# Kernel tuning notes

Measured on AMD Instinct MI355X. Metric: run time of the kernel, lower is better.

Reference implementation:

```python
import jax, jax.numpy as jnp
import numpy as np

IN = 128; HID = 128; OUT = 128; HEADS = 3; T1 = 0.2; T2 = 0.2
B = 512; L = 32; V = 100000; NMETA = 5


def _corr_full(s, t):
    # s, t: (B, L, E, N). Full cross-correlation along last axis.
    # Matches F.conv1d(hs, ht, groups=BLE, padding=N-1): out[k] = sum_m s[k+m-(N-1)] * t[m]
    N = s.shape[-1]
    sp = jnp.pad(s, ((0, 0), (0, 0), (0, 0), (N - 1, N - 1)))
    out = jnp.stack([(sp[..., k:k + N] * t).sum(-1) for k in range(2 * N - 1)], axis=-1)
    return jnp.swapaxes(out, -1, -2)  # (B, L, 2N-1, E)


def _node_att(h, Wt, Ws, Wc):
    # h: (B, L, P, E); Wt/Ws/Wc: (HEADS, E, HID)
    Bh, Lh, P, E = h.shape
    H = h.reshape(Bh * Lh, P, E)
    hi = jnp.einsum('ne,heo->hno', H[:, 0], Wt)                 # target-node projection
    logits = jnp.einsum('npe,heo,hno->hnp', H, Ws, hi) / T1     # (heads, BL, P)
    alpha = jax.nn.softmax(logits, axis=-1)                     # softmax over path positions
    Z = jnp.einsum('hnp,npe,heo->no', alpha, H, Wc) / HEADS     # mean over heads
    return Z.reshape(Bh, Lh, -1)


def _forward(emb_user, emb_item, emb_attr1, emb_attr2, emb_attr3, Wt, Ws, Wc,
             pw1, pb1, pw2, fw1, fb1, fw2, fb2,
             UI, IU, UIUI, IUIU, UIAI1, IAIU1, UIAI2, IAIU2, UIAI3, IAIU3):
    src = emb_user[UI[:, 0, 0]]
    tgt = emb_item[IU[:, 0, 0]]
    ui = jnp.stack([emb_user[UI[..., 0]], emb_item[UI[..., 1]]], axis=3)
    iu = jnp.stack([emb_item[IU[..., 0]], emb_user[IU[..., 1]]], axis=3)

    def p4(tabs, idx):
        return jnp.stack([tabs[k][idx[..., k]] for k in range(4)], axis=3)

    uiui = p4([emb_user, emb_item, emb_user, emb_item], UIUI)
    iuiu = p4([emb_item, emb_user, emb_item, emb_user], IUIU)
    uiai1 = p4([emb_user, emb_item, emb_attr1, emb_item], UIAI1)
    iaiu1 = p4([emb_item, emb_attr1, emb_item, emb_user], IAIU1)
    uiai2 = p4([emb_user, emb_item, emb_attr2, emb_item], UIAI2)
    iaiu2 = p4([emb_item, emb_attr2, emb_item, emb_user], IAIU2)
    uiai3 = p4([emb_user, emb_item, emb_attr3, emb_item], UIAI3)
    iaiu3 = p4([emb_item, emb_attr3, emb_item, emb_user], IAIU3)

    user_feats = [ui, uiui, uiai1, uiai2, uiai3]
    item_feats = [iu, iuiu, iaiu1, iaiu2, iaiu3]
    Hs = [_node_att(_corr_full(uf, itf), Wt[m], Ws[m], Wc[m])
          for m, (uf, itf) in enumerate(zip(user_feats, item_feats))]
    Z = jnp.stack(Hs, 1)                        # (B, 5, L, HID)
    z = Z.reshape(Z.shape[0], -1, HID)          # (B, 5L, HID)
    w = jnp.tanh(z @ pw1 + pb1) @ pw2 / T2      # (B, 5L, 1)
    beta = jax.nn.softmax(w, axis=1)
    path_out = (beta * z).sum(1)                # (B, HID)
    x = jnp.concatenate([src, tgt, path_out], axis=1)
    x = jax.nn.relu(x @ fw1 + fb1)              # dropout in eval mode -> identity
    return jax.nn.sigmoid(x @ fw2 + fb2)        # (B, 1)


def setup_inputs() -> dict:
    key = jax.random.key(0)
    ks = jax.random.split(key, 24)

    def idx(k, n):
        return jax.random.randint(k, (B, L, n), 0, V, dtype=jnp.int32)

    d = {
        'UI': idx(ks[0], 2), 'IU': idx(ks[1], 2),
        'UIUI': idx(ks[2], 4), 'IUIU': idx(ks[3], 4),
        'UIAI1': idx(ks[4], 4), 'IAIU1': idx(ks[5], 4),
        'UIAI2': idx(ks[6], 4), 'IAIU2': idx(ks[7], 4),
        'UIAI3': idx(ks[8], 4), 'IAIU3': idx(ks[9], 4),
    }

    def emb(k):
        t = jax.random.normal(k, (V + 1, IN), jnp.float32) * 0.05
        return t.at[0].set(0.0)  # padding_idx=0

    d['emb_user'] = emb(ks[10]); d['emb_item'] = emb(ks[11])
    d['emb_attr1'] = emb(ks[12]); d['emb_attr2'] = emb(ks[13]); d['emb_attr3'] = emb(ks[14])
    s = (2.0 / (IN + HID)) ** 0.5  # xavier scale
    d['Wt'] = jax.random.normal(ks[15], (NMETA, HEADS, IN, HID), jnp.float32) * s
    d['Ws'] = jax.random.normal(ks[16], (NMETA, HEADS, IN, HID), jnp.float32) * s
    d['Wc'] = jax.random.normal(ks[17], (NMETA, HEADS, IN, HID), jnp.float32) * s
    d['pw1'] = jax.random.normal(ks[18], (HID, HID), jnp.float32) * s
    d['pb1'] = jnp.zeros((HID,), jnp.float32)
    d['pw2'] = jax.random.normal(ks[19], (HID, 1), jnp.float32) * s
    d['fw1'] = jax.random.normal(ks[20], (3 * HID, OUT), jnp.float32) * 0.02
    d['fb1'] = jnp.zeros((OUT,), jnp.float32)
    d['fw2'] = jax.random.normal(ks[21], (OUT, 1), jnp.float32) * 0.02
    d['fb2'] = jnp.zeros((1,), jnp.float32)
    return d


def reference(UI, IU, UIUI, IUIU, UIAI1, IAIU1, UIAI2, IAIU2, UIAI3, IAIU3,
              emb_user, emb_item, emb_attr1, emb_attr2, emb_attr3,
              Wt, Ws, Wc, pw1, pb1, pw2, fw1, fb1, fw2, fb2):
    return _forward(emb_user, emb_item, emb_attr1, emb_attr2, emb_attr3, Wt, Ws, Wc,
                    pw1, pb1, pw2, fw1, fb1, fw2, fb2,
                    UI, IU, UIUI, IUIU, UIAI1, IAIU1, UIAI2, IAIU2, UIAI3, IAIU3)
```

## Files before the change

### kernel.cpp

```cpp
#include <hip/hip_runtime.h>
#include <hip/hip_bf16.h>
#include <cstdint>
#include <cstddef>


typedef __hip_bfloat16 bf16;
typedef __attribute__((ext_vector_type(8))) short  bfrag;
typedef __attribute__((ext_vector_type(4))) float  ffrag;

__device__ __forceinline__ float bflo(uint32_t u) { return __uint_as_float(u << 16); }
__device__ __forceinline__ float bfhi(uint32_t u) { return __uint_as_float(u & 0xffff0000u); }
__device__ __forceinline__ float bfs(unsigned short s) {
  return __uint_as_float(((uint32_t)s) << 16);
}
__device__ __forceinline__ uint16_t f2bfu(float x) {
  bf16 h = __float2bfloat16(x);
  return *(uint16_t*)&h;
}
__device__ __forceinline__ uint32_t pk2(float lo, float hi) {
  return (uint32_t)f2bfu(lo) | ((uint32_t)f2bfu(hi) << 16);
}

__global__ __launch_bounds__(256) void conv_emb(
    const float* __restrict__ a, const float* __restrict__ b,
    ushort* __restrict__ da, ushort* __restrict__ db, int n4)
{
  int stride = gridDim.x * 256;
  for (int i = blockIdx.x * 256 + threadIdx.x; i < 2 * n4; i += stride) {
    const float4* s; ushort* d; int j;
    if (i < n4) { s = (const float4*)a; d = da; j = i; }
    else        { s = (const float4*)b; d = db; j = i - n4; }
    float4 v = s[j];
    ushort4 o;
    o.x = f2bfu(v.x); o.y = f2bfu(v.y); o.z = f2bfu(v.z); o.w = f2bfu(v.w);
    ((ushort4*)d)[j] = o;
  }
}

__global__ __launch_bounds__(256) void prep_all(
    const float* __restrict__ Ws, const float* __restrict__ Wt,
    const float* __restrict__ Wc, const float* __restrict__ pw1,
    bf16* __restrict__ BmT, bf16* __restrict__ WcT, bf16* __restrict__ pw1T)
{
  int bid = blockIdx.x;
  int tid = threadIdx.x;
  if (bid < 240) {
    int mh = bid >> 4;
    int g  = bid & 15;
    int m = mh / 3, h = mh % 3;
    const float* ws = Ws + (size_t)mh * 16384;
    const float* wt = Wt + (size_t)mh * 16384;
    int e = tid & 127, half = tid >> 7;
    __shared__ float wtl[2][128];
    for (int ep0 = g * 8; ep0 < g * 8 + 8; ep0 += 2) {
      int ep = ep0 + half;
      wtl[half][e] = wt[ep * 128 + e];
      __syncthreads();
      float acc = 0.f;
      #pragma unroll 4
      for (int o = 0; o < 128; ++o) acc += ws[e * 128 + o] * wtl[half][o];
      BmT[((size_t)(m * 384 + h * 128 + e)) * 128 + ep] = __float2bfloat16(acc);
      __syncthreads();
    }
  } else if (bid < 1200) {
    int idx = (bid - 240) * 256 + tid;
    int he = idx % 384, mo = idx / 384;
    int m = mo >> 7, o = mo & 127;
    WcT[idx] = __float2bfloat16(Wc[((size_t)m * 384 + he) * 128 + o]);
  } else {
    int idx = (bid - 1200) * 256 + tid;
    int o = idx >> 7, k = idx & 127;
    pw1T[idx] = __float2bfloat16(pw1[(size_t)k * 128 + o]);
  }
}

template <int P, int UM, int TM>
__device__ __forceinline__ void metapath_body(
    char* smem,
    const void* Tu0, const void* Tu1, const void* Tu2, const void* Tu3,
    const void* Tt0, const void* Tt1, const void* Tt2, const void* Tt3,
    const int* __restrict__ idxU, const int* __restrict__ idxT,
    const bf16* __restrict__ BmT,
    const bf16* __restrict__ WcT,
    const bf16* __restrict__ pw1T,
    const float* __restrict__ pb1, const float* __restrict__ pw2,
    bf16* __restrict__ Zall, float* __restrict__ wbuf, int m, int tile)
{
  constexpr int PP = 2 * P - 1;
  constexpr int NS = PP * 136;
  bf16* Hs = (bf16*)smem;
  bf16* Ss = Hs + 16 * NS;
  bf16* Al = Ss + 16 * 392;
  float* wred = (float*)(Al + 16 * 24);

  int tid = threadIdx.x;
  int lane = tid & 63, wid = tid >> 6;
  int l15 = lane & 15, l4 = lane >> 4;
  int n0 = tile * 16;

  {
    const void* TU[4] = {Tu0, Tu1, Tu2, Tu3};
    const void* TT[4] = {Tt0, Tt1, Tt2, Tt3};
    int e = tid & 127;
    float su[4][P], st[4][P];
    #pragma unroll
    for (int g = 0; g < 4; ++g) {
      int n = n0 + g * 4 + (tid >> 7);
      #pragma unroll
      for (int p = 0; p < P; ++p) {
        size_t ou = (size_t)idxU[n * P + p] * 128 + e;
        size_t ot = (size_t)idxT[n * P + p] * 128 + e;
        su[g][p] = ((UM >> p) & 1) ? ((const float*)TU[p])[ou]
                                   : bfs(((const ushort*)TU[p])[ou]);
        st[g][p] = ((TM >> p) & 1) ? ((const float*)TT[p])[ot]
                                   : bfs(((const ushort*)TT[p])[ot]);
      }
    }
    #pragma unroll
    for (int g = 0; g < 4; ++g) {
      int ln = g * 4 + (tid >> 7);
      bf16* Hn = &Hs[ln * NS + e];
      #pragma unroll
      for (int k = 0; k < PP; ++k) {
        float acc = 0.f;
        #pragma unroll
        for (int i = 0; i < P; ++i) {
          int j = k + i - (P - 1);
          if (j >= 0 && j < P) acc += su[g][j] * st[g][i];
        }
        Hn[k * 136] = __float2bfloat16(acc);
      }
    }
  }
  __syncthreads();

  {
    bfrag a[4];
    #pragma unroll
    for (int kk = 0; kk < 4; ++kk)
      a[kk] = *(const bfrag*)&Hs[l15 * NS + kk * 32 + 8 * l4];
    #pragma unroll
    for (int f = 0; f < 3; ++f) {
      int col = wid * 48 + f * 16 + l15;
      ffrag acc = {0.f, 0.f, 0.f, 0.f};
      #pragma unroll
      for (int kk = 0; kk < 4; ++kk) {
        bfrag b = *(const bfrag*)&BmT[(size_t)col * 128 + kk * 32 + 8 * l4];
        acc = __builtin_amdgcn_mfma_f32_16x16x32_bf16(a[kk], b, acc, 0, 0, 0);
      }
      #pragma unroll
      for (int r = 0; r < 4; ++r) {
        int node = 4 * l4 + r;
        Ss[node * 392 + col] = __float2bfloat16(acc[r]);
      }
    }
  }
  __syncthreads();

  {
    int nd0 = wid * 2, nd1 = nd0 + 1;
    bool hi = (l15 >= 8);
    int nodeA = hi ? nd1 : nd0;
    int r15 = hi ? (l15 - 8) : l15;
    int ah = (r15 < 3) ? r15 : 2;
    int bp = (r15 < PP) ? r15 : (PP - 1);
    ffrag lacc = {0.f, 0.f, 0.f, 0.f};
    #pragma unroll
    for (int kk = 0; kk < 4; ++kk) {
      bfrag av = *(const bfrag*)&Ss[nodeA * 392 + ah * 128 + kk * 32 + 8 * l4];
      bfrag bv = *(const bfrag*)&Hs[nodeA * NS + bp * 136 + kk * 32 + 8 * l4];
      lacc = __builtin_amdgcn_mfma_f32_16x16x32_bf16(av, bv, lacc, 0, 0, 0);
    }
    bool val = ((l4 == 0) && !hi && (l15 < PP)) ||
               ((l4 == 2) &&  hi && (r15 < PP));
    float lg0 = val ? lacc[0] * 5.0f : -1e30f;
    float lg1 = val ? lacc[1] * 5.0f : -1e30f;
    float lg2 = val ? lacc[2] * 5.0f : -1e30f;
    float m0 = lg0, m1 = lg1, m2 = lg2;
    #pragma unroll
    for (int d = 1; d < 8; d <<= 1) {
      m0 = fmaxf(m0, __shfl_xor(m0, d));
      m1 = fmaxf(m1, __shfl_xor(m1, d));
      m2 = fmaxf(m2, __shfl_xor(m2, d));
    }
    float e0 = val ? __expf(lg0 - m0) : 0.f;
    float e1 = val ? __expf(lg1 - m1) : 0.f;
    float e2 = val ? __expf(lg2 - m2) : 0.f;
    float s0 = e0, s1 = e1, s2 = e2;
    #pragma unroll
    for (int d = 1; d < 8; d <<= 1) {
      s0 += __shfl_xor(s0, d);
      s1 += __shfl_xor(s1, d);
      s2 += __shfl_xor(s2, d);
    }
    if (val) {
      bf16* Aln = Al + nodeA * 24;
      Aln[r15]      = __float2bfloat16(e0 / s0);
      Aln[8 + r15]  = __float2bfloat16(e1 / s1);
      Aln[16 + r15] = __float2bfloat16(e2 / s2);
    }

    int node = tid >> 5, q = tid & 31;
    bfrag al0 = *(const bfrag*)&Al[node * 24];
    bfrag al1 = *(const bfrag*)&Al[node * 24 + 8];
    bfrag al2 = *(const bfrag*)&Al[node * 24 + 16];
    #pragma unroll
    for (int j = 0; j < 2; ++j) {
      int e2i = 4 * q + 2 * j;
      float a00 = 0.f, a01 = 0.f, a10 = 0.f, a11 = 0.f, a20 = 0.f, a21 = 0.f;
      #pragma unroll
      for (int pp = 0; pp < PP; ++pp) {
        uint32_t hv = *(const uint32_t*)&Hs[node * NS + pp * 136 + e2i];
        float lo = bflo(hv), hh = bfhi(hv);
        float f0 = bfs((unsigned short)al0[pp]);
        float f1 = bfs((unsigned short)al1[pp]);
        float f2 = bfs((unsigned short)al2[pp]);
        a00 += f0 * lo; a01 += f0 * hh;
        a10 += f1 * lo; a11 += f1 * hh;
        a20 += f2 * lo; a21 += f2 * hh;
      }
      *(uint32_t*)&Ss[node * 392 +       e2i] = pk2(a00, a01);
      *(uint32_t*)&Ss[node * 392 + 128 + e2i] = pk2(a10, a11);
      *(uint32_t*)&Ss[node * 392 + 256 + e2i] = pk2(a20, a21);
    }
  }
  __syncthreads();

  bf16* Zs = Hs;
  {
    bfrag a[12];
    #pragma unroll
    for (int kk = 0; kk < 12; ++kk)
      a[kk] = *(const bfrag*)&Ss[l15 * 392 + kk * 32 + 8 * l4];
    int col = wid * 16 + l15;
    ffrag acc = {0.f, 0.f, 0.f, 0.f};
    #pragma unroll
    for (int kk = 0; kk < 12; ++kk) {
      bfrag b = *(const bfrag*)&WcT[(size_t)col * 384 + kk * 32 + 8 * l4];
      acc = __builtin_amdgcn_mfma_f32_16x16x32_bf16(a[kk], b, acc, 0, 0, 0);
    }
    #pragma unroll
    for (int r = 0; r < 4; ++r) {
      int node = 4 * l4 + r;
      int gn = n0 + node;
      int crow = (((gn >> 5) * 5 + m) << 5) + (gn & 31);
      bf16 zb = __float2bfloat16(acc[r] * (1.0f / 3.0f));
      Zall[(size_t)crow * 128 + col] = zb;
      Zs[node * 136 + col] = zb;
    }
  }
  __syncthreads();

  {
    bfrag a5[4];
    #pragma unroll
    for (int kk = 0; kk < 4; ++kk)
      a5[kk] = *(const bfrag*)&Zs[l15 * 136 + kk * 32 + 8 * l4];
    int col = wid * 16 + l15;
    ffrag acc5 = {0.f, 0.f, 0.f, 0.f};
    #pragma unroll
    for (int kk = 0; kk < 4; ++kk) {
      bfrag b = *(const bfrag*)&pw1T[(size_t)col * 128 + kk * 32 + 8 * l4];
      acc5 = __builtin_amdgcn_mfma_f32_16x16x32_bf16(a5[kk], b, acc5, 0, 0, 0);
    }
    float bias = pb1[col], w2 = pw2[col];
    float part[4];
    #pragma unroll
    for (int r = 0; r < 4; ++r) part[r] = tanhf(acc5[r] + bias) * w2;
    #pragma unroll
    for (int d = 1; d < 16; d <<= 1) {
      #pragma unroll
      for (int r = 0; r < 4; ++r) part[r] += __shfl_xor(part[r], d);
    }
    if (l15 == 0) {
      #pragma unroll
      for (int r = 0; r < 4; ++r) wred[wid * 16 + 4 * l4 + r] = part[r];
    }
  }
  __syncthreads();
  if (tid < 16) {
    float s = 0.f;
    #pragma unroll
    for (int w = 0; w < 8; ++w) s += wred[w * 16 + tid];
    int gn = n0 + tid;
    int crow = (((gn >> 5) * 5 + m) << 5) + (gn & 31);
    wbuf[crow] = s * 5.0f;
  }
}

__global__ __launch_bounds__(512) void fused_all(
    const ushort* __restrict__ EU, const ushort* __restrict__ EI,
    const float* __restrict__ emb_a1, const float* __restrict__ emb_a2,
    const float* __restrict__ emb_a3,
    const int* __restrict__ UI,    const int* __restrict__ IU,
    const int* __restrict__ UIUI,  const int* __restrict__ IUIU,
    const int* __restrict__ UIAI1, const int* __restrict__ IAIU1,
    const int* __restrict__ UIAI2, const int* __restrict__ IAIU2,
    const int* __restrict__ UIAI3, const int* __restrict__ IAIU3,
    const bf16* __restrict__ BmT, const bf16* __restrict__ WcT,
    const bf16* __restrict__ pw1T,
    const float* __restrict__ pb1, const float* __restrict__ pw2,
    bf16* __restrict__ Zall, float* __restrict__ wbuf)
{
  extern __shared__ char smem[];
  int bid = blockIdx.x;
  int m = bid >> 10, tile = bid & 1023;
  if (m == 0) {
    metapath_body<2, 0, 0>(smem, EU, EI, nullptr, nullptr,
                           EI, EU, nullptr, nullptr,
                           UI, IU, BmT, WcT, pw1T, pb1, pw2,
                           Zall, wbuf, 0, tile);
  } else if (m == 1) {
    metapath_body<4, 0, 0>(smem, EU, EI, EU, EI,
                           EI, EU, EI, EU,
                           UIUI, IUIU,
                           BmT + (size_t)1 * 49152, WcT + (size_t)1 * 49152,
                           pw1T, pb1, pw2, Zall, wbuf, 1, tile);
  } else {
    const float* at = (m == 2) ? emb_a1 : (m == 3) ? emb_a2 : emb_a3;
    const int* iu_ = (m == 2) ? UIAI1 : (m == 3) ? UIAI2 : UIAI3;
    const int* it_ = (m == 2) ? IAIU1 : (m == 3) ? IAIU2 : IAIU3;
    metapath_body<4, 4, 2>(smem, EU, EI, at, EI,
                           EI, at, EI, EU,
                           iu_, it_,
                           BmT + (size_t)m * 49152, WcT + (size_t)m * 49152,
                           pw1T, pb1, pw2, Zall, wbuf, m, tile);
  }
}

__global__ __launch_bounds__(512) void fused_tail(
    const bf16* __restrict__ Zall,
    const float* __restrict__ wbuf,
    const int* __restrict__ UI, const int* __restrict__ IU,
    const float* __restrict__ emb_user, const float* __restrict__ emb_item,
    const float* __restrict__ fw1, const float* __restrict__ fb1,
    const float* __restrict__ fw2, const float* __restrict__ fb2,
    float* __restrict__ out)
{
  __shared__ bf16 Zs[160 * 136];
  __shared__ float wrow[160];
  __shared__ float ph[4][128];
  __shared__ float xs[384];
  __shared__ float sred[16];
  __shared__ float yred[2];

  int b = blockIdx.x, tid = threadIdx.x;
  int lane = tid & 63, wid = tid >> 6;

  {
    const float4* src = (const float4*)(Zall + (size_t)b * 160 * 128);
    float4 v[5];
    #pragma unroll
    for (int i = 0; i < 5; ++i) v[i] = src[i * 512 + tid];
    if (tid < 160) wrow[tid] = wbuf[b * 160 + tid];
    #pragma unroll
    for (int i = 0; i < 5; ++i) {
      int idx = i * 512 + tid;
      int row = idx >> 4, c8 = idx & 15;
      *(float4*)&Zs[row * 136 + c8 * 8] = v[i];
    }
  }
  __syncthreads();

  {
    float v = (tid < 160) ? wrow[tid] : -1e30f;
    #pragma unroll
    for (int off = 32; off; off >>= 1) v = fmaxf(v, __shfl_xor(v, off));
    if (lane == 0) sred[wid] = v;
    __syncthreads();
    if (tid < 64) {
      float mval = (lane < 8) ? sred[lane] : -1e30f;
      #pragma unroll
      for (int off = 4; off; off >>= 1) mval = fmaxf(mval, __shfl_xor(mval, off));
      if (lane == 0) sred[8] = mval;
    }
    __syncthreads();
    float mx = sred[8];
    float ev = (tid < 160) ? __expf(wrow[tid] - mx) : 0.f;
    float s = ev;
    #pragma unroll
    for (int off = 32; off; off >>= 1) s += __shfl_xor(s, off);
    if (lane == 0) sred[wid] = s;
    __syncthreads();
    if (tid < 64) {
      float sval = (lane < 8) ? sred[lane] : 0.f;
      #pragma unroll
      for (int off = 4; off; off >>= 1) sval += __shfl_xor(sval, off);
      if (lane == 0) sred[9] = sval;
    }
    __syncthreads();
    if (tid < 160) wrow[tid] = ev / sred[9];
  }
  __syncthreads();

  {
    int e = tid & 127, q = tid >> 7;
    float acc = 0.f;
    #pragma unroll 4
    for (int j = q * 40; j < q * 40 + 40; ++j)
      acc += wrow[j] * __bfloat162float(Zs[j * 136 + e]);
    ph[q][e] = acc;
  }
  __syncthreads();

  {
    int su = UI[b * 64];
    int ti = IU[b * 64];
    if (tid < 128) {
      xs[256 + tid] = ph[0][tid] + ph[1][tid] + ph[2][tid] + ph[3][tid];
    } else if (tid < 256) {
      xs[tid - 128] = emb_user[(size_t)su * 128 + (tid - 128)];
    } else if (tid < 384) {
      xs[tid - 128] = emb_item[(size_t)ti * 128 + (tid - 256)];
    }
  }
  __syncthreads();

  {
    int o = tid & 127, q = tid >> 7;
    float acc = 0.f;
    #pragma unroll 4
    for (int i = q * 96; i < q * 96 + 96; ++i)
      acc += xs[i] * fw1[(size_t)i * 128 + o];
    __syncthreads();
    ph[q][o] = acc;
  }
  __syncthreads();
  if (tid < 128) {
    float y = fmaxf(ph[0][tid] + ph[1][tid] + ph[2][tid] + ph[3][tid] + fb1[tid],
                    0.0f) * fw2[tid];
    #pragma unroll
    for (int off = 32; off; off >>= 1) y += __shfl_down(y, off);
    if ((tid & 63) == 0) yred[tid >> 6] = y;
  }
  __syncthreads();
  if (tid == 0) {
    float s = yred[0] + yred[1] + fb2[0];
    out[b] = 1.0f / (1.0f + expf(-s));
  }
}

extern "C" void kernel_launch(void* const* d_in, const int* in_sizes, int n_in,
                              void* d_out, int out_size, void* d_ws, size_t ws_size,
                              hipStream_t stream)
{
  const int* UI    = (const int*)d_in[0];
  const int* IU    = (const int*)d_in[1];
  const int* UIUI  = (const int*)d_in[2];
  const int* IUIU  = (const int*)d_in[3];
  const int* UIAI1 = (const int*)d_in[4];
  const int* IAIU1 = (const int*)d_in[5];
  const int* UIAI2 = (const int*)d_in[6];
  const int* IAIU2 = (const int*)d_in[7];
  const int* UIAI3 = (const int*)d_in[8];
  const int* IAIU3 = (const int*)d_in[9];
  const float* emb_user = (const float*)d_in[10];
  const float* emb_item = (const float*)d_in[11];
  const float* emb_a1   = (const float*)d_in[12];
  const float* emb_a2   = (const float*)d_in[13];
  const float* emb_a3   = (const float*)d_in[14];
  const float* Wt  = (const float*)d_in[15];
  const float* Ws  = (const float*)d_in[16];
  const float* Wc  = (const float*)d_in[17];
  const float* pw1 = (const float*)d_in[18];
  const float* pb1 = (const float*)d_in[19];
  const float* pw2 = (const float*)d_in[20];
  const float* fw1 = (const float*)d_in[21];
  const float* fb1 = (const float*)d_in[22];
  const float* fw2 = (const float*)d_in[23];
  const float* fb2 = (const float*)d_in[24];
  float* out = (float*)d_out;

  char* wsb = (char*)d_ws;
  bf16*   BmT  = (bf16*)wsb;
  bf16*   WcT  = (bf16*)(wsb + 491520);
  bf16*   pw1T = (bf16*)(wsb + 983040);
  bf16*   Zall = (bf16*)(wsb + 1015808);
  float*  wbuf = (float*)(wsb + 21987328);
  ushort* EU16 = (ushort*)(wsb + 22315008);
  ushort* EI16 = (ushort*)(wsb + 47915264);

  int n4 = (100001 * 128) / 4;
  conv_emb<<<8192, 256, 0, stream>>>(emb_user, emb_item, EU16, EI16, n4);
  prep_all<<<1264, 256, 0, stream>>>(Ws, Wt, Wc, pw1, BmT, WcT, pw1T);

  fused_all<<<5120, 512, 44288, stream>>>(
      EU16, EI16, emb_a1, emb_a2, emb_a3,
      UI, IU, UIUI, IUIU, UIAI1, IAIU1, UIAI2, IAIU2, UIAI3, IAIU3,
      BmT, WcT, pw1T, pb1, pw2, Zall, wbuf);

  fused_tail<<<512, 512, 0, stream>>>(Zall, wbuf,
                                      UI, IU, emb_user, emb_item,
                                      fw1, fb1, fw2, fb2, out);
}
```

Baseline: 225.7 us.

## Process two tiles per block and prefetch second tile's gather during first compute

Each block of the fused metapath kernel now handles two consecutive 16-node tiles, and the grid is halved to match. The embedding gathers for the second tile are issued into registers before the first tile's MFMA and attention compute, so their global-memory latency can overlap with that compute. The gathered values are kept as raw bits and converted to float only when the correlation is written to shared memory. The cost is extra live registers across the compute phase, which risks spills or lower occupancy, plus fewer blocks in the grid.

After: 215.0 us. 1.05x faster.

```diff
diff --git a/kernel.cpp b/kernel.cpp
--- a/kernel.cpp
+++ b/kernel.cpp
@@ -75,13 +75,64 @@
 }
 
 template <int P, int UM, int TM>
-__device__ __forceinline__ void metapath_body(
+__device__ __forceinline__ void gather_issue(
+    const void* const* TU, const void* const* TT,
+    const int* __restrict__ idxU, const int* __restrict__ idxT,
+    int n0, int tid, uint32_t (&su)[4][P], uint32_t (&st)[4][P])
+{
+  int e = tid & 127;
+  #pragma unroll
+  for (int g = 0; g < 4; ++g) {
+    int n = n0 + g * 4 + (tid >> 7);
+    #pragma unroll
+    for (int p = 0; p < P; ++p) {
+      size_t ou = (size_t)idxU[n * P + p] * 128 + e;
+      size_t ot = (size_t)idxT[n * P + p] * 128 + e;
+      su[g][p] = ((UM >> p) & 1) ? __float_as_uint(((const float*)TU[p])[ou])
+                                 : (uint32_t)((const ushort*)TU[p])[ou];
+      st[g][p] = ((TM >> p) & 1) ? __float_as_uint(((const float*)TT[p])[ot])
+                                 : (uint32_t)((const ushort*)TT[p])[ot];
+    }
+  }
+}
+
+template <int P, int UM, int TM>
+__device__ __forceinline__ void corr_store(
+    bf16* __restrict__ Hs, const uint32_t (&su)[4][P],
+    const uint32_t (&st)[4][P], int tid)
+{
+  constexpr int PP = 2 * P - 1;
+  constexpr int NS = PP * 136;
+  int e = tid & 127;
+  #pragma unroll
+  for (int g = 0; g < 4; ++g) {
+    int ln = g * 4 + (tid >> 7);
+    float fu[P], ft[P];
+    #pragma unroll
+    for (int p = 0; p < P; ++p) {
+      fu[p] = ((UM >> p) & 1) ? __uint_as_float(su[g][p])
+                              : __uint_as_float(su[g][p] << 16);
+      ft[p] = ((TM >> p) & 1) ? __uint_as_float(st[g][p])
+                              : __uint_as_float(st[g][p] << 16);
+    }
+    bf16* Hn = &Hs[ln * NS + e];
+    #pragma unroll
+    for (int k = 0; k < PP; ++k) {
+      float acc = 0.f;
+      #pragma unroll
+      for (int i = 0; i < P; ++i) {
+        int j = k + i - (P - 1);
+        if (j >= 0 && j < P) acc += fu[j] * ft[i];
+      }
+      Hn[k * 136] = __float2bfloat16(acc);
+    }
+  }
+}
+
+template <int P>
+__device__ __forceinline__ void compute_tile(
     char* smem,
-    const void* Tu0, const void* Tu1, const void* Tu2, const void* Tu3,
-    const void* Tt0, const void* Tt1, const void* Tt2, const void* Tt3,
-    const int* __restrict__ idxU, const int* __restrict__ idxT,
-    const bf16* __restrict__ BmT,
-    const bf16* __restrict__ WcT,
+    const bf16* __restrict__ BmT, const bf16* __restrict__ WcT,
     const bf16* __restrict__ pw1T,
     const float* __restrict__ pb1, const float* __restrict__ pw2,
     bf16* __restrict__ Zall, float* __restrict__ wbuf, int m, int tile)
@@ -97,42 +148,6 @@
   int lane = tid & 63, wid = tid >> 6;
   int l15 = lane & 15, l4 = lane >> 4;
   int n0 = tile * 16;
-
-  {
-    const void* TU[4] = {Tu0, Tu1, Tu2, Tu3};
-    const void* TT[4] = {Tt0, Tt1, Tt2, Tt3};
-    int e = tid & 127;
-    float su[4][P], st[4][P];
-    #pragma unroll
-    for (int g = 0; g < 4; ++g) {
-      int n = n0 + g * 4 + (tid >> 7);
-      #pragma unroll
-      for (int p = 0; p < P; ++p) {
-        size_t ou = (size_t)idxU[n * P + p] * 128 + e;
-        size_t ot = (size_t)idxT[n * P + p] * 128 + e;
-        su[g][p] = ((UM >> p) & 1) ? ((const float*)TU[p])[ou]
-                                   : bfs(((const ushort*)TU[p])[ou]);
-        st[g][p] = ((TM >> p) & 1) ? ((const float*)TT[p])[ot]
-                                   : bfs(((const ushort*)TT[p])[ot]);
-      }
-    }
-    #pragma unroll
-    for (int g = 0; g < 4; ++g) {
-      int ln = g * 4 + (tid >> 7);
-      bf16* Hn = &Hs[ln * NS + e];
-      #pragma unroll
-      for (int k = 0; k < PP; ++k) {
-        float acc = 0.f;
-        #pragma unroll
-        for (int i = 0; i < P; ++i) {
-          int j = k + i - (P - 1);
-          if (j >= 0 && j < P) acc += su[g][j] * st[g][i];
-        }
-        Hn[k * 136] = __float2bfloat16(acc);
-      }
-    }
-  }
-  __syncthreads();
 
   {
     bfrag a[4];
@@ -288,6 +303,39 @@
   }
 }
 
+template <int P, int UM, int TM>
+__device__ __forceinline__ void pipeline_body(
+    char* smem,
+    const void* Tu0, const void* Tu1, const void* Tu2, const void* Tu3,
+    const void* Tt0, const void* Tt1, const void* Tt2, const void* Tt3,
+    const int* __restrict__ idxU, const int* __restrict__ idxT,
+    const bf16* __restrict__ BmT, const bf16* __restrict__ WcT,
+    const bf16* __restrict__ pw1T,
+    const float* __restrict__ pb1, const float* __restrict__ pw2,
+    bf16* __restrict__ Zall, float* __restrict__ wbuf, int m, int pair)
+{
+  const void* TU[4] = {Tu0, Tu1, Tu2, Tu3};
+  const void* TT[4] = {Tt0, Tt1, Tt2, Tt3};
+  bf16* Hs = (bf16*)smem;
+  int tid = threadIdx.x;
+  int t0 = pair * 2, t1 = t0 + 1;
+
+  uint32_t su0[4][P], st0[4][P];
+  gather_issue<P, UM, TM>(TU, TT, idxU, idxT, t0 * 16, tid, su0, st0);
+  corr_store<P, UM, TM>(Hs, su0, st0, tid);
+  __syncthreads();
+
+  uint32_t su1[4][P], st1[4][P];
+  gather_issue<P, UM, TM>(TU, TT, idxU, idxT, t1 * 16, tid, su1, st1);
+
+  compute_tile<P>(smem, BmT, WcT, pw1T, pb1, pw2, Zall, wbuf, m, t0);
+
+  corr_store<P, UM, TM>(Hs, su1, st1, tid);
+  __syncthreads();
+
+  compute_tile<P>(smem, BmT, WcT, pw1T, pb1, pw2, Zall, wbuf, m, t1);
+}
+
 __global__ __launch_bounds__(512) void fused_all(
     const ushort* __restrict__ EU, const ushort* __restrict__ EI,
     const float* __restrict__ emb_a1, const float* __restrict__ emb_a2,
@@ -304,27 +352,27 @@
 {
   extern __shared__ char smem[];
   int bid = blockIdx.x;
-  int m = bid >> 10, tile = bid & 1023;
+  int m = bid >> 9, pair = bid & 511;
   if (m == 0) {
-    metapath_body<2, 0, 0>(smem, EU, EI, nullptr, nullptr,
+    pipeline_body<2, 0, 0>(smem, EU, EI, nullptr, nullptr,
                            EI, EU, nullptr, nullptr,
                            UI, IU, BmT, WcT, pw1T, pb1, pw2,
-                           Zall, wbuf, 0, tile);
+                           Zall, wbuf, 0, pair);
   } else if (m == 1) {
-    metapath_body<4, 0, 0>(smem, EU, EI, EU, EI,
+    pipeline_body<4, 0, 0>(smem, EU, EI, EU, EI,
                            EI, EU, EI, EU,
                            UIUI, IUIU,
                            BmT + (size_t)1 * 49152, WcT + (size_t)1 * 49152,
-                           pw1T, pb1, pw2, Zall, wbuf, 1, tile);
+                           pw1T, pb1, pw2, Zall, wbuf, 1, pair);
   } else {
     const float* at = (m == 2) ? emb_a1 : (m == 3) ? emb_a2 : emb_a3;
     const int* iu_ = (m == 2) ? UIAI1 : (m == 3) ? UIAI2 : UIAI3;
     const int* it_ = (m == 2) ? IAIU1 : (m == 3) ? IAIU2 : IAIU3;
-    metapath_body<4, 4, 2>(smem, EU, EI, at, EI,
+    pipeline_body<4, 4, 2>(smem, EU, EI, at, EI,
                            EI, at, EI, EU,
                            iu_, it_,
                            BmT + (size_t)m * 49152, WcT + (size_t)m * 49152,
-                           pw1T, pb1, pw2, Zall, wbuf, m, tile);
+                           pw1T, pb1, pw2, Zall, wbuf, m, pair);
   }
 }
 
@@ -484,7 +532,7 @@
   conv_emb<<<8192, 256, 0, stream>>>(emb_user, emb_item, EU16, EI16, n4);
   prep_all<<<1264, 256, 0, stream>>>(Ws, Wt, Wc, pw1, BmT, WcT, pw1T);
 
-  fused_all<<<5120, 512, 44288, stream>>>(
+  fused_all<<<2560, 512, 44288, stream>>>(
       EU16, EI16, emb_a1, emb_a2, emb_a3,
       UI, IU, UIUI, IUIU, UIAI1, IAIU1, UIAI2, IAIU2, UIAI3, IAIU3,
       BmT, WcT, pw1T, pb1, pw2, Zall, wbuf);
```
